# Kernel tuning notes

Hardware: AMD Instinct MI355X
Metric: run time of the kernel (lower is better)

Reference implementation:

```python
import jax, jax.numpy as jnp
import numpy as np


def _moie_block(x, w, b, alpha, activation):
    # x: [B, in], w: [K, in, out], b: [K, out], alpha: [B, K]
    z = jnp.einsum('bi,kio->bko', x, w) + b          # [B, K, out] per-expert outputs
    combined = jnp.einsum('bko,bk->bo', z, alpha)    # alpha-weighted sum over experts
    if activation:
        combined = jax.nn.relu(combined)
    return combined


def setup_inputs() -> dict:
    key = jax.random.key(0)
    ks = jax.random.split(key, 8)
    B, D, K, H = 16384, 512, 8, 512
    s = 0.02  # weight init scale
    return {
        'x': jax.random.normal(ks[0], (B, D), jnp.float32),
        'gate_w': jax.random.normal(ks[1], (D, K), jnp.float32) * s,
        'gate_b': jnp.zeros((K,), jnp.float32),
        'w0': jax.random.normal(ks[2], (K, D, H), jnp.float32) * s,
        'b0': jnp.zeros((K, H), jnp.float32),
        'w1': jax.random.normal(ks[3], (K, H, H), jnp.float32) * s,
        'b1': jnp.zeros((K, H), jnp.float32),
        'w2': jax.random.normal(ks[4], (K, H, H), jnp.float32) * s,
        'b2': jnp.zeros((K, H), jnp.float32),
        'wo': jax.random.normal(ks[5], (K, H, D), jnp.float32) * s,
        'bo': jnp.zeros((K, D), jnp.float32),
    }


def reference(x, gate_w, gate_b, w0, b0, w1, b1, w2, b2, wo, bo):
    # Gating: softmax(Linear(x)) -> alpha [B, K]; same alpha reused at every layer.
    alpha = jax.nn.softmax(x @ gate_w + gate_b, axis=-1)
    # n_blocks=3 hidden MoIE blocks: MoIEBlock (no act) -> ReLU -> Dropout(0, eval=identity)
    h = _moie_block(x, w0, b0, alpha, activation=True)
    h = _moie_block(h, w1, b1, alpha, activation=True)
    h = _moie_block(h, w2, b2, alpha, activation=True)
    # Output MoIEBlock: no activation
    return _moie_block(h, wo, bo, alpha, activation=False)
```

## Files before the change

### kernel.cpp

```cpp
#include <hip/hip_runtime.h>
#include <stdint.h>

typedef _Float16 f16;
typedef _Float16 f16x8 __attribute__((ext_vector_type(8)));
typedef float f32x4 __attribute__((ext_vector_type(4)));

#define NROWS 16384
#define DIM   512
#define NEXP  8
#define BM    128
#define BN    128
#define BK    32
#define NKS   16
#define WSTRIDE (DIM*DIM)

#define GLOAD16(gp, lp) __builtin_amdgcn_global_load_lds( \
    (const __attribute__((address_space(1))) void*)(gp),  \
    (__attribute__((address_space(3))) void*)(lp), 16, 0, 0)

#define MFMA16(a,b,c) __builtin_amdgcn_mfma_f32_16x16x32_f16(a, b, c, 0, 0, 0)

#define WAITV(N) asm volatile("s_waitcnt vmcnt(" #N ")" ::: "memory")
#define BAR()    __builtin_amdgcn_s_barrier()

__global__ __launch_bounds__(256) void convert_w(
    const float* __restrict__ w0, const float* __restrict__ w1,
    const float* __restrict__ w2, const float* __restrict__ wo,
    f16* __restrict__ Wt)
{
    __shared__ float tile[32][33];
    int b  = blockIdx.x;
    int m  = b >> 8;
    int bi = (b >> 4) & 15;
    int bj = b & 15;
    int layer = m >> 3;
    const float* src =
        (layer == 0 ? w0 : layer == 1 ? w1 : layer == 2 ? w2 : wo)
        + (size_t)(m & 7) * DIM * DIM;
    f16* dst = Wt + (size_t)m * DIM * DIM;
    int tx = threadIdx.x & 31, ty = threadIdx.x >> 5;
#pragma unroll
    for (int r = 0; r < 4; ++r)
        tile[ty + 8*r][tx] = src[(size_t)(bi*32 + ty + 8*r) * DIM + bj*32 + tx];
    __syncthreads();
#pragma unroll
    for (int r = 0; r < 4; ++r)
        dst[(size_t)(bj*32 + ty + 8*r) * DIM + bi*32 + tx] = (f16)tile[tx][ty + 8*r];
}

__global__ __launch_bounds__(256) void gate_kernel(
    const float* __restrict__ x, const float* __restrict__ gw,
    const float* __restrict__ gb, float* __restrict__ alpha,
    f16* __restrict__ xh)
{
    int tid = threadIdx.x, lane = tid & 63, wid = tid >> 6;
    int row = blockIdx.x * 4 + wid;
    const float* xr = x + (size_t)row * DIM;
    float acc[8] = {0,0,0,0,0,0,0,0};
    float xv[8];
#pragma unroll
    for (int j = 0; j < 8; ++j) {
        int d = lane + 64*j;
        float v = xr[d];
        xv[j] = v;
        const float4* g = (const float4*)(gw + (size_t)d * 8);
        float4 g0 = g[0], g1 = g[1];
        acc[0] += v*g0.x; acc[1] += v*g0.y; acc[2] += v*g0.z; acc[3] += v*g0.w;
        acc[4] += v*g1.x; acc[5] += v*g1.y; acc[6] += v*g1.z; acc[7] += v*g1.w;
    }
#pragma unroll
    for (int mlane = 32; mlane >= 1; mlane >>= 1) {
#pragma unroll
        for (int k = 0; k < 8; ++k) acc[k] += __shfl_xor(acc[k], mlane, 64);
    }
#pragma unroll
    for (int k = 0; k < 8; ++k) acc[k] += gb[k];
    float mx = acc[0];
#pragma unroll
    for (int k = 1; k < 8; ++k) mx = fmaxf(mx, acc[k]);
    float s = 0.f;
#pragma unroll
    for (int k = 0; k < 8; ++k) { acc[k] = __expf(acc[k] - mx); s += acc[k]; }
    float inv = 1.0f / s;
    if (lane == 0) {
        float4 a0 = {acc[0]*inv, acc[1]*inv, acc[2]*inv, acc[3]*inv};
        float4 a1 = {acc[4]*inv, acc[5]*inv, acc[6]*inv, acc[7]*inv};
        *(float4*)(alpha + (size_t)row*8)     = a0;
        *(float4*)(alpha + (size_t)row*8 + 4) = a1;
    }
#pragma unroll
    for (int j = 0; j < 8; ++j)
        xh[(size_t)row * DIM + lane + 64*j] = (f16)xv[j];
}


#define READ_BF(SLOT) \
      bf0 = *(const f16x8*)(Ball + (SLOT)*4096 + bOff); \
      bf1 = *(const f16x8*)(Ball + (SLOT)*4096 + bOff + 512); \
      bf2 = *(const f16x8*)(Ball + (SLOT)*4096 + bOff + 1024); \
      bf3 = *(const f16x8*)(Ball + (SLOT)*4096 + bOff + 1536);

#define READ_AF(P) \
      af0 = *(const f16x8*)((P) + aOff); \
      af1 = *(const f16x8*)((P) + aOff + 512); \
      af2 = *(const f16x8*)((P) + aOff + 1024); \
      af3 = *(const f16x8*)((P) + aOff + 1536);

#define MULS(E) { \
      f16 s0_ = salh0[E], s1_ = salh1[E], s2_ = salh2[E], s3_ = salh3[E]; \
      a0 = af0 * (f16x8){s0_,s0_,s0_,s0_,s0_,s0_,s0_,s0_}; \
      a1 = af1 * (f16x8){s1_,s1_,s1_,s1_,s1_,s1_,s1_,s1_}; \
      a2 = af2 * (f16x8){s2_,s2_,s2_,s2_,s2_,s2_,s2_,s2_}; \
      a3 = af3 * (f16x8){s3_,s3_,s3_,s3_,s3_,s3_,s3_,s3_}; }

#define MFMAS() \
      __builtin_amdgcn_s_setprio(1); \
      acc[0][0]=MFMA16(a0,bf0,acc[0][0]); acc[0][1]=MFMA16(a0,bf1,acc[0][1]); \
      acc[0][2]=MFMA16(a0,bf2,acc[0][2]); acc[0][3]=MFMA16(a0,bf3,acc[0][3]); \
      acc[1][0]=MFMA16(a1,bf0,acc[1][0]); acc[1][1]=MFMA16(a1,bf1,acc[1][1]); \
      acc[1][2]=MFMA16(a1,bf2,acc[1][2]); acc[1][3]=MFMA16(a1,bf3,acc[1][3]); \
      acc[2][0]=MFMA16(a2,bf0,acc[2][0]); acc[2][1]=MFMA16(a2,bf1,acc[2][1]); \
      acc[2][2]=MFMA16(a2,bf2,acc[2][2]); acc[2][3]=MFMA16(a2,bf3,acc[2][3]); \
      acc[3][0]=MFMA16(a3,bf0,acc[3][0]); acc[3][1]=MFMA16(a3,bf1,acc[3][1]); \
      acc[3][2]=MFMA16(a3,bf2,acc[3][2]); acc[3][3]=MFMA16(a3,bf3,acc[3][3]); \
      __builtin_amdgcn_s_setprio(0);

#define STG_B(KS, EXP, SLOT) \
      GLOAD16(bSrc + (size_t)(EXP)*WSTRIDE + (KS)*BK,          bD + (SLOT)*4096); \
      GLOAD16(bSrc + (size_t)(EXP)*WSTRIDE + (KS)*BK + 64*DIM, bD + (SLOT)*4096 + 2048);
#define STG_A(KS, DST) \
      GLOAD16(aSrc + (KS)*BK,          DST); \
      GLOAD16(aSrc + (KS)*BK + 64*DIM, DST + 2048);

#define PHX(WAITN, SLOT, E, ISSUE) \
    asm volatile("s_waitcnt vmcnt(" #WAITN ")" ::: "memory"); \
    READ_BF(SLOT) \
    MULS(E) \
    __builtin_amdgcn_s_barrier(); \
    MFMAS() \
    ISSUE

#define PH0(WAITN, ARD, ISSUE) \
    asm volatile("s_waitcnt vmcnt(" #WAITN ")" ::: "memory"); \
    READ_AF(ARD); \
    READ_BF(0) \
    __builtin_amdgcn_s_barrier(); \
    MULS(0) \
    MFMAS() \
    ISSUE

template<int RELU, int OUTF32>
__global__ __launch_bounds__(256, 2) void moie_gemm(
    const f16*  __restrict__ A,
    const f16*  __restrict__ Wt,
    const float* __restrict__ alpha,
    const float* __restrict__ bias,
    f16*  __restrict__ Hout,
    float* __restrict__ Fout)
{
    __shared__ __align__(16) f16 Abuf[2][BM*BK];
    __shared__ __align__(16) f16 Bbuf[4][BN*BK];
    __shared__ float alpha_s[BM*9];
    __shared__ float bias_s[NEXP*BN];

    int bid = blockIdx.x;
    int swz = (bid & 7) * 64 + (bid >> 3);
    int cb = swz >> 7, rb = swz & 127;
    int rowBase = rb * BM, colBase = cb * BN;
    int tid = threadIdx.x, lane = tid & 63, wid = tid >> 6;
    int wm = wid >> 1, wn = wid & 1;

    for (int i = tid; i < BM*NEXP; i += 256)
        alpha_s[(i >> 3)*9 + (i & 7)] = alpha[(size_t)(rowBase + (i >> 3))*8 + (i & 7)];
    for (int i = tid; i < NEXP*BN; i += 256)
        bias_s[i] = bias[(i >> 7)*DIM + colBase + (i & 127)];

    int srow = tid >> 2;
    int sg   = ((tid & 3) ^ ((srow >> 1) & 3)) * 8;
    const f16* aSrc = A  + (size_t)(rowBase + srow) * DIM + sg;
    const f16* bSrc = Wt + (size_t)(colBase + srow) * DIM + sg;
    f16* aW0 = Abuf[0] + tid*8;
    f16* aW1 = Abuf[1] + tid*8;
    f16* bD  = Bbuf[0] + tid*8;
    const f16* Ball = Bbuf[0];

    int kg   = ((lane >> 4) ^ (((lane & 15) >> 1) & 3)) * 8;
    int aOff = (wm*64 + (lane & 15)) * BK + kg;
    int bOff = (wn*64 + (lane & 15)) * BK + kg;

    __syncthreads();

    STG_A(0, aW0);
    STG_B(0, 0, 0); STG_B(0, 1, 1); STG_B(0, 2, 2); STG_B(0, 3, 3);

    f16 salh0[NEXP], salh1[NEXP], salh2[NEXP], salh3[NEXP];
    {
        int r0 = wm*64 + (lane & 15);
#pragma unroll
        for (int e = 0; e < NEXP; ++e) {
            salh0[e] = (f16)alpha_s[(r0     )*9 + e];
            salh1[e] = (f16)alpha_s[(r0 + 16)*9 + e];
            salh2[e] = (f16)alpha_s[(r0 + 32)*9 + e];
            salh3[e] = (f16)alpha_s[(r0 + 48)*9 + e];
        }
    }

    f16x8 af0, af1, af2, af3, a0, a1, a2, a3, bf0, bf1, bf2, bf3;
    f32x4 acc[4][4];
#pragma unroll
    for (int i = 0; i < 4; ++i)
#pragma unroll
        for (int j = 0; j < 4; ++j) acc[i][j] = (f32x4){0.f,0.f,0.f,0.f};

    WAITV(4); BAR();

    for (int ss = 0; ss < NKS - 1; ++ss) {
        const f16* Ard = (ss & 1) ? Abuf[1] : Abuf[0];
        f16* an = (ss & 1) ? aW0 : aW1;
        PH0(4, Ard, { STG_B(ss, 4, 0); STG_A(ss + 1, an); })
        PHX(6, 1, 1, { STG_B(ss, 5, 1); })
        PHX(6, 2, 2, { STG_B(ss, 6, 2); })
        PHX(4, 3, 3, { STG_B(ss, 7, 3); })
        PHX(4, 0, 4, { STG_B(ss + 1, 0, 0); })
        PHX(4, 1, 5, { STG_B(ss + 1, 1, 1); })
        PHX(4, 2, 6, { STG_B(ss + 1, 2, 2); })
        PHX(4, 3, 7, { STG_B(ss + 1, 3, 3); })
    }
    {
        PH0(4, Abuf[1], { STG_B(15, 4, 0); })
        PHX(4, 1, 1, { STG_B(15, 5, 1); })
        PHX(4, 2, 2, { STG_B(15, 6, 2); })
        PHX(4, 3, 3, { STG_B(15, 7, 3); })
        PHX(4, 0, 4, { })
        PHX(2, 1, 5, { })
        PHX(0, 2, 6, { })
        PHX(0, 3, 7, { })
    }

#pragma unroll
    for (int i = 0; i < 4; ++i)
#pragma unroll
        for (int q = 0; q < 4; ++q) {
            int rloc = wm*64 + i*16 + (lane >> 4)*4 + q;
            size_t row = (size_t)(rowBase + rloc);
#pragma unroll
            for (int j = 0; j < 4; ++j) {
                int cloc = wn*64 + j*16 + (lane & 15);
                float v = acc[i][j][q];
#pragma unroll
                for (int e2 = 0; e2 < NEXP; ++e2)
                    v += alpha_s[rloc*9 + e2] * bias_s[e2*BN + cloc];
                if (RELU) v = fmaxf(v, 0.f);
                if (OUTF32) Fout[row*DIM + colBase + cloc] = v;
                else        Hout[row*DIM + colBase + cloc] = (f16)v;
            }
        }
}

extern "C" void kernel_launch(void* const* d_in, const int* in_sizes, int n_in,
                              void* d_out, int out_size, void* d_ws, size_t ws_size,
                              hipStream_t stream)
{
    const float* x  = (const float*)d_in[0];
    const float* gw = (const float*)d_in[1];
    const float* gb = (const float*)d_in[2];
    const float* w0 = (const float*)d_in[3];
    const float* b0 = (const float*)d_in[4];
    const float* w1 = (const float*)d_in[5];
    const float* b1 = (const float*)d_in[6];
    const float* w2 = (const float*)d_in[7];
    const float* b2 = (const float*)d_in[8];
    const float* wo = (const float*)d_in[9];
    const float* bo = (const float*)d_in[10];
    float* out = (float*)d_out;

    char* ws = (char*)d_ws;
    const size_t wtBytes = (size_t)4 * NEXP * DIM * DIM * sizeof(f16);
    f16*   Wt    = (f16*)ws;
    float* alpha = (float*)(ws + wtBytes);
    f16*   h0    = (f16*)(ws + wtBytes + (size_t)NROWS*NEXP*sizeof(float));
    f16*   h1    = h0 + (size_t)NROWS * DIM;
    const size_t L = (size_t)NEXP * DIM * DIM;

    convert_w<<<8192, 256, 0, stream>>>(w0, w1, w2, wo, Wt);
    gate_kernel<<<NROWS/4, 256, 0, stream>>>(x, gw, gb, alpha, h0);

    moie_gemm<1,0><<<512, 256, 0, stream>>>(h0, Wt,       alpha, b0, h1, nullptr);
    moie_gemm<1,0><<<512, 256, 0, stream>>>(h1, Wt + L,   alpha, b1, h0, nullptr);
    moie_gemm<1,0><<<512, 256, 0, stream>>>(h0, Wt + 2*L, alpha, b2, h1, nullptr);
    moie_gemm<0,1><<<512, 256, 0, stream>>>(h1, Wt + 3*L, alpha, bo, nullptr, out);
}
```

Measured before the change: 312.4 us.

## Halve GEMM row tile to 64 and use triple-buffered weight slots

Shrinks the per-block row tile from 128 to 64, which doubles the grid to 1024 blocks and halves the accumulator and A-fragment registers. The weight staging ring drops from four slots to three, so the phase schedule is rewritten as a 3-way unrolled rotation with adjusted waitcnt values. The goal is better occupancy and load balance across CUs. The cost is that each weight tile is now reused by fewer rows, so total weight traffic from L2 roughly doubles and each load is covered by less MFMA work.

```diff
diff --git a/kernel.cpp b/kernel.cpp
--- a/kernel.cpp
+++ b/kernel.cpp
@@ -8,7 +8,7 @@
 #define NROWS 16384
 #define DIM   512
 #define NEXP  8
-#define BM    128
+#define BM    64
 #define BN    128
 #define BK    32
 #define NKS   16
@@ -102,16 +102,12 @@
 
 #define READ_AF(P) \
       af0 = *(const f16x8*)((P) + aOff); \
-      af1 = *(const f16x8*)((P) + aOff + 512); \
-      af2 = *(const f16x8*)((P) + aOff + 1024); \
-      af3 = *(const f16x8*)((P) + aOff + 1536);
+      af1 = *(const f16x8*)((P) + aOff + 512);
 
 #define MULS(E) { \
-      f16 s0_ = salh0[E], s1_ = salh1[E], s2_ = salh2[E], s3_ = salh3[E]; \
+      f16 s0_ = salh0[E], s1_ = salh1[E]; \
       a0 = af0 * (f16x8){s0_,s0_,s0_,s0_,s0_,s0_,s0_,s0_}; \
-      a1 = af1 * (f16x8){s1_,s1_,s1_,s1_,s1_,s1_,s1_,s1_}; \
-      a2 = af2 * (f16x8){s2_,s2_,s2_,s2_,s2_,s2_,s2_,s2_}; \
-      a3 = af3 * (f16x8){s3_,s3_,s3_,s3_,s3_,s3_,s3_,s3_}; }
+      a1 = af1 * (f16x8){s1_,s1_,s1_,s1_,s1_,s1_,s1_,s1_}; }
 
 #define MFMAS() \
       __builtin_amdgcn_s_setprio(1); \
@@ -119,18 +115,13 @@
       acc[0][2]=MFMA16(a0,bf2,acc[0][2]); acc[0][3]=MFMA16(a0,bf3,acc[0][3]); \
       acc[1][0]=MFMA16(a1,bf0,acc[1][0]); acc[1][1]=MFMA16(a1,bf1,acc[1][1]); \
       acc[1][2]=MFMA16(a1,bf2,acc[1][2]); acc[1][3]=MFMA16(a1,bf3,acc[1][3]); \
-      acc[2][0]=MFMA16(a2,bf0,acc[2][0]); acc[2][1]=MFMA16(a2,bf1,acc[2][1]); \
-      acc[2][2]=MFMA16(a2,bf2,acc[2][2]); acc[2][3]=MFMA16(a2,bf3,acc[2][3]); \
-      acc[3][0]=MFMA16(a3,bf0,acc[3][0]); acc[3][1]=MFMA16(a3,bf1,acc[3][1]); \
-      acc[3][2]=MFMA16(a3,bf2,acc[3][2]); acc[3][3]=MFMA16(a3,bf3,acc[3][3]); \
       __builtin_amdgcn_s_setprio(0);
 
 #define STG_B(KS, EXP, SLOT) \
       GLOAD16(bSrc + (size_t)(EXP)*WSTRIDE + (KS)*BK,          bD + (SLOT)*4096); \
       GLOAD16(bSrc + (size_t)(EXP)*WSTRIDE + (KS)*BK + 64*DIM, bD + (SLOT)*4096 + 2048);
 #define STG_A(KS, DST) \
-      GLOAD16(aSrc + (KS)*BK,          DST); \
-      GLOAD16(aSrc + (KS)*BK + 64*DIM, DST + 2048);
+      GLOAD16(aSrc + (KS)*BK, DST);
 
 #define PHX(WAITN, SLOT, E, ISSUE) \
     asm volatile("s_waitcnt vmcnt(" #WAITN ")" ::: "memory"); \
@@ -140,14 +131,26 @@
     MFMAS() \
     ISSUE
 
-#define PH0(WAITN, ARD, ISSUE) \
+#define PH0(WAITN, SLOT, ARD, ISSUE) \
     asm volatile("s_waitcnt vmcnt(" #WAITN ")" ::: "memory"); \
     READ_AF(ARD); \
-    READ_BF(0) \
+    READ_BF(SLOT) \
     __builtin_amdgcn_s_barrier(); \
     MULS(0) \
     MFMAS() \
     ISSUE
+
+#define SSBODY(SS, S0,S1,S2,S3,S4,S5,S6,S7) { \
+      const f16* Ard = ((SS) & 1) ? Abuf[1] : Abuf[0]; \
+      f16* an = ((SS) & 1) ? aW0 : aW1; \
+      PH0(4, S0, Ard, { STG_B(SS, 3, S0); STG_A((SS) + 1, an); }) \
+      PHX(5, S1, 1, { STG_B(SS, 4, S1); }) \
+      PHX(5, S2, 2, { STG_B(SS, 5, S2); }) \
+      PHX(5, S3, 3, { STG_B(SS, 6, S3); }) \
+      PHX(4, S4, 4, { STG_B(SS, 7, S4); }) \
+      PHX(4, S5, 5, { STG_B((SS) + 1, 0, S5); }) \
+      PHX(4, S6, 6, { STG_B((SS) + 1, 1, S6); }) \
+      PHX(4, S7, 7, { STG_B((SS) + 1, 2, S7); }) }
 
 template<int RELU, int OUTF32>
 __global__ __launch_bounds__(256, 2) void moie_gemm(
@@ -159,13 +162,13 @@
     float* __restrict__ Fout)
 {
     __shared__ __align__(16) f16 Abuf[2][BM*BK];
-    __shared__ __align__(16) f16 Bbuf[4][BN*BK];
+    __shared__ __align__(16) f16 Bbuf[3][BN*BK];
     __shared__ float alpha_s[BM*9];
     __shared__ float bias_s[NEXP*BN];
 
     int bid = blockIdx.x;
-    int swz = (bid & 7) * 64 + (bid >> 3);
-    int cb = swz >> 7, rb = swz & 127;
+    int swz = (bid & 7) * 128 + (bid >> 3);
+    int cb = swz >> 8, rb = swz & 255;
     int rowBase = rb * BM, colBase = cb * BN;
     int tid = threadIdx.x, lane = tid & 63, wid = tid >> 6;
     int wm = wid >> 1, wn = wid & 1;
@@ -185,63 +188,54 @@
     const f16* Ball = Bbuf[0];
 
     int kg   = ((lane >> 4) ^ (((lane & 15) >> 1) & 3)) * 8;
-    int aOff = (wm*64 + (lane & 15)) * BK + kg;
+    int aOff = (wm*32 + (lane & 15)) * BK + kg;
     int bOff = (wn*64 + (lane & 15)) * BK + kg;
 
     __syncthreads();
 
     STG_A(0, aW0);
-    STG_B(0, 0, 0); STG_B(0, 1, 1); STG_B(0, 2, 2); STG_B(0, 3, 3);
-
-    f16 salh0[NEXP], salh1[NEXP], salh2[NEXP], salh3[NEXP];
+    STG_B(0, 0, 0); STG_B(0, 1, 1); STG_B(0, 2, 2);
+
+    f16 salh0[NEXP], salh1[NEXP];
     {
-        int r0 = wm*64 + (lane & 15);
+        int r0 = wm*32 + (lane & 15);
 #pragma unroll
         for (int e = 0; e < NEXP; ++e) {
             salh0[e] = (f16)alpha_s[(r0     )*9 + e];
             salh1[e] = (f16)alpha_s[(r0 + 16)*9 + e];
-            salh2[e] = (f16)alpha_s[(r0 + 32)*9 + e];
-            salh3[e] = (f16)alpha_s[(r0 + 48)*9 + e];
         }
     }
 
-    f16x8 af0, af1, af2, af3, a0, a1, a2, a3, bf0, bf1, bf2, bf3;
-    f32x4 acc[4][4];
-#pragma unroll
-    for (int i = 0; i < 4; ++i)
+    f16x8 af0, af1, a0, a1, bf0, bf1, bf2, bf3;
+    f32x4 acc[2][4];
+#pragma unroll
+    for (int i = 0; i < 2; ++i)
 #pragma unroll
         for (int j = 0; j < 4; ++j) acc[i][j] = (f32x4){0.f,0.f,0.f,0.f};
 
     WAITV(4); BAR();
 
-    for (int ss = 0; ss < NKS - 1; ++ss) {
-        const f16* Ard = (ss & 1) ? Abuf[1] : Abuf[0];
-        f16* an = (ss & 1) ? aW0 : aW1;
-        PH0(4, Ard, { STG_B(ss, 4, 0); STG_A(ss + 1, an); })
-        PHX(6, 1, 1, { STG_B(ss, 5, 1); })
-        PHX(6, 2, 2, { STG_B(ss, 6, 2); })
-        PHX(4, 3, 3, { STG_B(ss, 7, 3); })
-        PHX(4, 0, 4, { STG_B(ss + 1, 0, 0); })
-        PHX(4, 1, 5, { STG_B(ss + 1, 1, 1); })
-        PHX(4, 2, 6, { STG_B(ss + 1, 2, 2); })
-        PHX(4, 3, 7, { STG_B(ss + 1, 3, 3); })
+    for (int ss = 0; ss < NKS - 1; ss += 3) {
+        SSBODY(ss,     0,1,2,0,1,2,0,1)
+        SSBODY(ss + 1, 2,0,1,2,0,1,2,0)
+        SSBODY(ss + 2, 1,2,0,1,2,0,1,2)
     }
     {
-        PH0(4, Abuf[1], { STG_B(15, 4, 0); })
-        PHX(4, 1, 1, { STG_B(15, 5, 1); })
-        PHX(4, 2, 2, { STG_B(15, 6, 2); })
-        PHX(4, 3, 3, { STG_B(15, 7, 3); })
-        PHX(4, 0, 4, { })
-        PHX(2, 1, 5, { })
-        PHX(0, 2, 6, { })
-        PHX(0, 3, 7, { })
-    }
-
-#pragma unroll
-    for (int i = 0; i < 4; ++i)
+        PH0(4, 0, Abuf[1], { STG_B(15, 3, 0); })
+        PHX(4, 1, 1, { STG_B(15, 4, 1); })
+        PHX(4, 2, 2, { STG_B(15, 5, 2); })
+        PHX(4, 0, 3, { STG_B(15, 6, 0); })
+        PHX(4, 1, 4, { STG_B(15, 7, 1); })
+        PHX(4, 2, 5, { })
+        PHX(2, 0, 6, { })
+        PHX(0, 1, 7, { })
+    }
+
+#pragma unroll
+    for (int i = 0; i < 2; ++i)
 #pragma unroll
         for (int q = 0; q < 4; ++q) {
-            int rloc = wm*64 + i*16 + (lane >> 4)*4 + q;
+            int rloc = wm*32 + i*16 + (lane >> 4)*4 + q;
             size_t row = (size_t)(rowBase + rloc);
 #pragma unroll
             for (int j = 0; j < 4; ++j) {
@@ -285,8 +279,8 @@
     convert_w<<<8192, 256, 0, stream>>>(w0, w1, w2, wo, Wt);
     gate_kernel<<<NROWS/4, 256, 0, stream>>>(x, gw, gb, alpha, h0);
 
-    moie_gemm<1,0><<<512, 256, 0, stream>>>(h0, Wt,       alpha, b0, h1, nullptr);
-    moie_gemm<1,0><<<512, 256, 0, stream>>>(h1, Wt + L,   alpha, b1, h0, nullptr);
-    moie_gemm<1,0><<<512, 256, 0, stream>>>(h0, Wt + 2*L, alpha, b2, h1, nullptr);
-    moie_gemm<0,1><<<512, 256, 0, stream>>>(h1, Wt + 3*L, alpha, bo, nullptr, out);
-}
+    moie_gemm<1,0><<<1024, 256, 0, stream>>>(h0, Wt,       alpha, b0, h1, nullptr);
+    moie_gemm<1,0><<<1024, 256, 0, stream>>>(h1, Wt + L,   alpha, b1, h0, nullptr);
+    moie_gemm<1,0><<<1024, 256, 0, stream>>>(h0, Wt + 2*L, alpha, b2, h1, nullptr);
+    moie_gemm<0,1><<<1024, 256, 0, stream>>>(h1, Wt + 3*L, alpha, bo, nullptr, out);
+}
```

Measured after the change: 461.8 us. +47.8%, slower.
